# Kernel tuning notes

Measured on AMD Instinct MI355X. Metric: run time of the kernel, lower is better.

Reference implementation:

```python
import jax, jax.numpy as jnp
import numpy as np

H = 768       # hidden_size
NH = 12       # num_attention_heads
HD = H // NH  # head_size
FF = 3072     # intermediate_size
EPS = 1e-5


def _layernorm(x, g, b):
    m = jnp.mean(x, axis=-1, keepdims=True)
    v = jnp.var(x, axis=-1, keepdims=True)
    return (x - m) * jax.lax.rsqrt(v + EPS) * g + b


def setup_inputs() -> dict:
    key = jax.random.key(0)
    ks = jax.random.split(key, 12)
    B, Sq, Skv = 8, 1024, 1024
    s = 0.02
    return {
        "freq_hidden_states": jax.random.normal(ks[0], (B, Sq, H), jnp.float32),
        "image_hidden_states": jax.random.normal(ks[1], (B, Skv, H), jnp.float32),
        # attention projections (stored [in, out])
        "Wq": jax.random.normal(ks[2], (H, H), jnp.float32) * s,
        "bq": jnp.zeros((H,), jnp.float32),
        "Wk": jax.random.normal(ks[3], (H, H), jnp.float32) * s,
        "bk": jnp.zeros((H,), jnp.float32),
        "Wv": jax.random.normal(ks[4], (H, H), jnp.float32) * s,
        "bv": jnp.zeros((H,), jnp.float32),
        # layernorms
        "ln_att_g": jnp.ones((H,), jnp.float32),
        "ln_att_b": jnp.zeros((H,), jnp.float32),
        "ln_mlp_g": jnp.ones((H,), jnp.float32),
        "ln_mlp_b": jnp.zeros((H,), jnp.float32),
        # MLP
        "W1": jax.random.normal(ks[5], (H, FF), jnp.float32) * s,
        "b1": jnp.zeros((FF,), jnp.float32),
        "W2": jax.random.normal(ks[6], (FF, H), jnp.float32) * s,
        "b2": jnp.zeros((H,), jnp.float32),
    }


def reference(image_hidden_states, freq_hidden_states, Wq, bq, Wk, bk, Wv, bv,
              ln_att_g, ln_att_b, ln_mlp_g, ln_mlp_b, W1, b1, W2, b2):
    B, Sq, _ = freq_hidden_states.shape
    Skv = image_hidden_states.shape[1]
    # cross-attention: query from freq, key/value from image
    q = (freq_hidden_states @ Wq + bq).reshape(B, Sq, NH, HD)
    k = (image_hidden_states @ Wk + bk).reshape(B, Skv, NH, HD)
    v = (image_hidden_states @ Wv + bv).reshape(B, Skv, NH, HD)
    scores = jnp.einsum("bqhd,bkhd->bhqk", q, k) / jnp.sqrt(jnp.float32(HD))
    probs = jax.nn.softmax(scores, axis=-1)
    ctx = jnp.einsum("bhqk,bkhd->bqhd", probs, v).reshape(B, Sq, H)
    # residual with post-LN on the attention output
    h = freq_hidden_states + _layernorm(ctx, ln_att_g, ln_att_b)
    # MLP + residual with post-LN on the MLP output
    mlp = jax.nn.relu(h @ W1 + b1) @ W2 + b2
    return h + _layernorm(mlp, ln_mlp_g, ln_mlp_b)
```

## Files before the change

kernel.cpp:

```cpp
#include <hip/hip_runtime.h>
#include <hip/hip_bf16.h>

#define H 768
#define NH 12
#define HD 64
#define FF 3072
#define SQ 1024
#define SKV 1024

typedef __hip_bfloat16 bf16;
typedef __attribute__((ext_vector_type(8))) short short8;
typedef __attribute__((ext_vector_type(4))) float f32x4;

__device__ inline void gload16(const void* g, void* l) {
  __builtin_amdgcn_global_load_lds((const __attribute__((address_space(1))) void*)g,
                                   (__attribute__((address_space(3))) void*)l, 16, 0, 0);
}

__device__ inline float bf2f(unsigned short u) {
  unsigned int x = ((unsigned int)u) << 16;
  return __builtin_bit_cast(float, x);
}

__device__ inline void cvt_body(const float* __restrict__ src, bf16* __restrict__ dst, int blk) {
  int i = blk * 256 + threadIdx.x;
  float4 v = ((const float4*)src)[i];
  union { unsigned short u[4]; uint2 q; } o;
  bf16 t0 = __float2bfloat16(v.x); o.u[0] = *(unsigned short*)&t0;
  bf16 t1 = __float2bfloat16(v.y); o.u[1] = *(unsigned short*)&t1;
  bf16 t2 = __float2bfloat16(v.z); o.u[2] = *(unsigned short*)&t2;
  bf16 t3 = __float2bfloat16(v.w); o.u[3] = *(unsigned short*)&t3;
  ((uint2*)dst)[i] = o.q;
}

__device__ inline void trans_body(const float* __restrict__ src, bf16* __restrict__ dst,
                                  int Kd, int Nd, int blk, float* tile ) {
  int ntx = Nd >> 5;
  int n0 = (blk % ntx) << 5, k0 = (blk / ntx) << 5;
  int tx = threadIdx.x & 31, ty = threadIdx.x >> 5;
#pragma unroll
  for (int i = 0; i < 4; ++i)
    tile[(ty + i * 8) * 33 + tx] = src[(size_t)(k0 + ty + i * 8) * Nd + n0 + tx];
  __syncthreads();
#pragma unroll
  for (int i = 0; i < 4; ++i)
    dst[(size_t)(n0 + ty + i * 8) * Kd + k0 + tx] = __float2bfloat16(tile[tx * 33 + ty + i * 8]);
}

__global__ __launch_bounds__(256) void prep(
    const float* freq, const float* image, bf16* freqb, bf16* imageb,
    const float* Wq, const float* Wk, const float* Wv, const float* W1, const float* W2,
    bf16* WTq, bf16* WTk, bf16* WTv, bf16* W1T, bf16* W2T, int c1) {
  __shared__ float tile[32 * 33];
  int b = blockIdx.x;
  if (b < c1) { cvt_body(freq, freqb, b); return; }
  b -= c1;
  if (b < c1) { cvt_body(image, imageb, b); return; }
  b -= c1;
  const int TQ = (H / 32) * (H / 32);
  const int T1 = (FF / 32) * (H / 32);
  if (b < TQ)            { trans_body(Wq, WTq, H, H, b, tile); return; }
  b -= TQ;
  if (b < TQ)            { trans_body(Wk, WTk, H, H, b, tile); return; }
  b -= TQ;
  if (b < TQ)            { trans_body(Wv, WTv, H, H, b, tile); return; }
  b -= TQ;
  if (b < T1)            { trans_body(W1, W1T, H, FF, b, tile); return; }
  b -= T1;
  trans_body(W2, W2T, FF, H, b, tile);
}

template <int EPI, int BN>
__global__ __launch_bounds__(256) void gemm_bt(
    const bf16* __restrict__ A, const bf16* __restrict__ BT,
    const float* __restrict__ bias0, const float* __restrict__ bias1,
    void* __restrict__ out0, void* __restrict__ out1, int M, int N, int K) {
  constexpr int SI = BN / 32;
  constexpr int JF = BN / 32;
  __shared__ __align__(16) bf16 lA[128 * 64];
  __shared__ __align__(16) bf16 lB[BN * 64];
  const int t = threadIdx.x;
  const int lane = t & 63, w = t >> 6;
  const int wr = w >> 1, wc = w & 1;
  const int nt = N / BN;
  const int nwg = gridDim.x;
  int bid = blockIdx.x;
  int logical = ((nwg & 7) == 0) ? ((bid & 7) * (nwg >> 3) + (bid >> 3)) : bid;
  const int m0 = (logical / nt) << 7;
  const int n0 = (logical % nt) * BN;

  const f32x4 fz = {0.f, 0.f, 0.f, 0.f};
  f32x4 acc[4][JF];
#pragma unroll
  for (int i = 0; i < 4; ++i)
#pragma unroll
    for (int j = 0; j < JF; ++j) acc[i][j] = fz;

  for (int kt = 0; kt < K; kt += 64) {
#pragma unroll
    for (int i = 0; i < 4; ++i) {
      int idx = i * 256 + t;
      int row = idx >> 3;
      int chunk = (idx & 7) ^ (row & 7);
      gload16(A + (size_t)(m0 + row) * K + kt + chunk * 8, lA + (size_t)(i * 256 + w * 64) * 8);
    }
#pragma unroll
    for (int i = 0; i < SI; ++i) {
      int idx = i * 256 + t;
      int row = idx >> 3;
      int chunk = (idx & 7) ^ (row & 7);
      gload16(BT + (size_t)(n0 + row) * K + kt + chunk * 8, lB + (size_t)(i * 256 + w * 64) * 8);
    }
    __syncthreads();

    short8 af[2][4], bfv[2][JF];
#pragma unroll
    for (int s = 0; s < 2; ++s) {
#pragma unroll
      for (int i = 0; i < 4; ++i) {
        int ra = wr * 64 + i * 16 + (lane & 15);
        int ca = (s * 4 + (lane >> 4)) ^ (ra & 7);
        af[s][i] = *(const short8*)&lA[ra * 64 + ca * 8];
      }
#pragma unroll
      for (int j = 0; j < JF; ++j) {
        int rb = wc * (BN / 2) + j * 16 + (lane & 15);
        int cb = (s * 4 + (lane >> 4)) ^ (rb & 7);
        bfv[s][j] = *(const short8*)&lB[rb * 64 + cb * 8];
      }
    }
#pragma unroll
    for (int s = 0; s < 2; ++s)
#pragma unroll
      for (int i = 0; i < 4; ++i)
#pragma unroll
        for (int j = 0; j < JF; ++j)
          acc[i][j] = __builtin_amdgcn_mfma_f32_16x16x32_bf16(af[s][i], bfv[s][j], acc[i][j], 0, 0, 0);
    __syncthreads();
  }

#pragma unroll
  for (int i = 0; i < 4; ++i) {
    int mbase = m0 + wr * 64 + i * 16 + ((lane >> 4) << 2);
#pragma unroll
    for (int j = 0; j < JF; ++j) {
      int n = n0 + wc * (BN / 2) + j * 16 + (lane & 15);
#pragma unroll
      for (int r = 0; r < 4; ++r) {
        int m = mbase + r;
        float v = acc[i][j][r];
        if (EPI == 0) {
          v = (v + bias0[n]) * 0.180336880f;
          int hlin = (m >> 10) * NH + (n >> 6);
          ((bf16*)out0)[((size_t)hlin * SQ + (m & 1023)) * HD + (n & 63)] = __float2bfloat16(v);
        } else if (EPI == 1) {
          int sel = (n >= H);
          int nn = n - (sel ? H : 0);
          v += (sel ? bias1 : bias0)[nn];
          int hlin = (m >> 10) * NH + (nn >> 6);
          if (!sel)
            ((bf16*)out0)[((size_t)hlin * SKV + (m & 1023)) * HD + (nn & 63)] = __float2bfloat16(v);
          else
            ((bf16*)out1)[((size_t)hlin * HD + (nn & 63)) * SKV + (m & 1023)] = __float2bfloat16(v);
        } else if (EPI == 2) {
          v += bias0[n];
          v = fmaxf(v, 0.f);
          ((bf16*)out0)[(size_t)m * N + n] = __float2bfloat16(v);
        } else {
          v += bias0[n];
          ((bf16*)out0)[(size_t)m * N + n] = __float2bfloat16(v);
        }
      }
    }
  }
}

__global__ __launch_bounds__(512, 4) void attn_fwd(
    const bf16* __restrict__ Q,
    const bf16* __restrict__ Kg_,
    const bf16* __restrict__ VT,
    bf16* __restrict__ ctx, int nblk) {
  __shared__ __align__(16) bf16 Ks[2][64 * 64];
  __shared__ __align__(16) bf16 Vs[2][64 * 64];
  __shared__ __align__(16) bf16 PQ[8 * 16 * 72];

  const int t = threadIdx.x, lane = t & 63, w = t >> 6;
  int bid = blockIdx.x;
  int logical = ((nblk & 7) == 0) ? (bid & 7) * (nblk >> 3) + (bid >> 3) : bid;
  const int hl = logical >> 3;
  const int q0 = (logical & 7) << 7;
  const bf16* Qg = Q + ((size_t)hl * SQ + q0) * HD;
  const bf16* Kg = Kg_ + (size_t)hl * SKV * HD;
  const bf16* Vg = VT + (size_t)hl * HD * SKV;

#pragma unroll
  for (int rep = 0; rep < 2; ++rep) {
    int idx = rep * 512 + t;
    int row = idx >> 3;
    int chunk = (idx & 7) ^ (row & 7);
    gload16(Qg + (size_t)row * HD + chunk * 8, PQ + (size_t)(rep * 512 + w * 64) * 8);
  }
  {
    int row = t >> 3, chunk = (t & 7) ^ (row & 7);
    gload16(Kg + (size_t)row * HD + chunk * 8, &Ks[0][(size_t)w * 64 * 8]);
    gload16(Vg + (size_t)row * SKV + chunk * 8, &Vs[0][(size_t)w * 64 * 8]);
  }
  __syncthreads();

  short8 aq[2];
#pragma unroll
  for (int s = 0; s < 2; ++s) {
    int row = w * 16 + (lane & 15);
    int chunk = (s * 4 + (lane >> 4)) ^ (row & 7);
    aq[s] = *(const short8*)&PQ[row * 64 + chunk * 8];
  }
  __syncthreads();

  float l_r[4];
#pragma unroll
  for (int r = 0; r < 4; ++r) l_r[r] = 0.f;
  const f32x4 fz = {0.f, 0.f, 0.f, 0.f};
  f32x4 oacc[4];
#pragma unroll
  for (int j = 0; j < 4; ++j) oacc[j] = fz;

  bf16* Pw = PQ + w * (16 * 72);
  const short s1 = (short)0x3F80;
  const short8 ones = {s1, s1, s1, s1, s1, s1, s1, s1};

#pragma unroll 2
  for (int i = 0; i < 16; ++i) {
    const int buf = i & 1;
    if (i < 15) {
      int kvn = (i + 1) << 6;
      int row = t >> 3, chunk = (t & 7) ^ (row & 7);
      gload16(Kg + (size_t)(kvn + row) * HD + chunk * 8, &Ks[buf ^ 1][(size_t)w * 64 * 8]);
      gload16(Vg + (size_t)row * SKV + kvn + chunk * 8, &Vs[buf ^ 1][(size_t)w * 64 * 8]);
    }

    f32x4 sa[4];
#pragma unroll
    for (int n = 0; n < 4; ++n) sa[n] = fz;
    __builtin_amdgcn_s_setprio(1);
#pragma unroll
    for (int s = 0; s < 2; ++s)
#pragma unroll
      for (int n = 0; n < 4; ++n) {
        int rb = n * 16 + (lane & 15);
        int cb = (s * 4 + (lane >> 4)) ^ (rb & 7);
        short8 bk = *(const short8*)&Ks[buf][rb * 64 + cb * 8];
        sa[n] = __builtin_amdgcn_mfma_f32_16x16x32_bf16(aq[s], bk, sa[n], 0, 0, 0);
      }
    __builtin_amdgcn_s_setprio(0);

#pragma unroll
    for (int n = 0; n < 4; ++n)
#pragma unroll
      for (int r = 0; r < 4; ++r)
        Pw[(((lane >> 4) << 2) + r) * 72 + n * 16 + (lane & 15)] =
            __float2bfloat16(exp2f(sa[n][r]));

    f32x4 ld = fz;
    __builtin_amdgcn_s_setprio(1);
#pragma unroll
    for (int kk = 0; kk < 2; ++kk) {
      short8 pa = *(const short8*)&Pw[(lane & 15) * 72 + kk * 32 + ((lane >> 4) << 3)];
      ld = __builtin_amdgcn_mfma_f32_16x16x32_bf16(pa, ones, ld, 0, 0, 0);
#pragma unroll
      for (int j = 0; j < 4; ++j) {
        int rb = j * 16 + (lane & 15);
        int cb = (kk * 4 + (lane >> 4)) ^ (rb & 7);
        short8 bv = *(const short8*)&Vs[buf][rb * 64 + cb * 8];
        oacc[j] = __builtin_amdgcn_mfma_f32_16x16x32_bf16(pa, bv, oacc[j], 0, 0, 0);
      }
    }
    __builtin_amdgcn_s_setprio(0);
#pragma unroll
    for (int r = 0; r < 4; ++r) l_r[r] += ld[r];

    __syncthreads();
  }

  const int b = hl / NH, hh = hl % NH;
  float rl[4];
#pragma unroll
  for (int r = 0; r < 4; ++r) rl[r] = 1.0f / l_r[r];
#pragma unroll
  for (int j = 0; j < 4; ++j)
#pragma unroll
    for (int r = 0; r < 4; ++r) {
      int q = q0 + w * 16 + ((lane >> 4) << 2) + r;
      int d = j * 16 + (lane & 15);
      ctx[((size_t)b * SQ + q) * H + hh * HD + d] = __float2bfloat16(oacc[j][r] * rl[r]);
    }
}

__global__ __launch_bounds__(192) void ln_res(
    const bf16* __restrict__ x, const float* __restrict__ res,
    const float* __restrict__ g, const float* __restrict__ beta,
    float* __restrict__ o32, bf16* __restrict__ ob, int write_b) {
  const int row = blockIdx.x;
  const int t = threadIdx.x;
  float v[4];
  float s = 0.f, s2 = 0.f;
  ushort4 xv = ((const ushort4*)(x + (size_t)row * H))[t];
  v[0] = bf2f(xv.x); v[1] = bf2f(xv.y); v[2] = bf2f(xv.z); v[3] = bf2f(xv.w);
#pragma unroll
  for (int k = 0; k < 4; ++k) { s += v[k]; s2 += v[k] * v[k]; }
#pragma unroll
  for (int off = 32; off > 0; off >>= 1) {
    s += __shfl_down(s, off);
    s2 += __shfl_down(s2, off);
  }
  __shared__ float red[8];
  if ((t & 63) == 0) { red[t >> 6] = s; red[4 + (t >> 6)] = s2; }
  __syncthreads();
  float st = red[0] + red[1] + red[2];
  float s2t = red[4] + red[5] + red[6];
  float mean = st * (1.f / 768.f);
  float var = s2t * (1.f / 768.f) - mean * mean;
  float rs = rsqrtf(var + 1e-5f);
  {
    float4 rv = ((const float4*)(res + (size_t)row * H))[t];
    float4 gv = ((const float4*)g)[t];
    float4 bv = ((const float4*)beta)[t];
    float4 o;
    o.x = rv.x + (v[0] - mean) * rs * gv.x + bv.x;
    o.y = rv.y + (v[1] - mean) * rs * gv.y + bv.y;
    o.z = rv.z + (v[2] - mean) * rs * gv.z + bv.z;
    o.w = rv.w + (v[3] - mean) * rs * gv.w + bv.w;
    ((float4*)(o32 + (size_t)row * H))[t] = o;
    if (write_b) {
      union { unsigned short u[4]; uint2 q; } ob4;
      bf16 b0 = __float2bfloat16(o.x); ob4.u[0] = *(unsigned short*)&b0;
      bf16 b1 = __float2bfloat16(o.y); ob4.u[1] = *(unsigned short*)&b1;
      bf16 b2 = __float2bfloat16(o.z); ob4.u[2] = *(unsigned short*)&b2;
      bf16 b3 = __float2bfloat16(o.w); ob4.u[3] = *(unsigned short*)&b3;
      ((uint2*)(ob + (size_t)row * H))[t] = ob4.q;
    }
  }
}

extern "C" void kernel_launch(void* const* d_in, const int* in_sizes, int n_in,
                              void* d_out, int out_size, void* d_ws, size_t ws_size,
                              hipStream_t stream) {
  const float* freq  = (const float*)d_in[0];
  const float* image = (const float*)d_in[1];
  const float* Wq = (const float*)d_in[2];
  const float* bq = (const float*)d_in[3];
  const float* Wk = (const float*)d_in[4];
  const float* bk = (const float*)d_in[5];
  const float* Wv = (const float*)d_in[6];
  const float* bv = (const float*)d_in[7];
  const float* g1 = (const float*)d_in[8];
  const float* be1 = (const float*)d_in[9];
  const float* g2 = (const float*)d_in[10];
  const float* be2 = (const float*)d_in[11];
  const float* W1 = (const float*)d_in[12];
  const float* b1 = (const float*)d_in[13];
  const float* W2 = (const float*)d_in[14];
  const float* b2 = (const float*)d_in[15];

  const int Bc = in_sizes[0] / (SQ * H);
  const int M = Bc * SQ;

  char* p = (char*)d_ws;
  bf16* W1T = (bf16*)p;  p += (size_t)FF * H * 2;
  bf16* W2T = (bf16*)p;  p += (size_t)H * FF * 2;
  bf16* ctxb = (bf16*)p; p += (size_t)M * H * 2;
  float* h32 = (float*)p; p += (size_t)M * H * 4;
  bf16* hb = (bf16*)p;   p += (size_t)M * H * 2;
  char* U = p;
  bf16* freqb = (bf16*)U;
  bf16* imageb = (bf16*)(U + (size_t)M * H * 2);
  bf16* WTq   = (bf16*)(U + (size_t)2 * M * H * 2);
  bf16* WTkv  = (bf16*)(U + (size_t)2 * M * H * 2 + (size_t)H * H * 2);
  bf16* Qb    = (bf16*)(U + (size_t)2 * M * H * 2 + (size_t)3 * H * H * 2);
  bf16* Kbuf  = (bf16*)((char*)Qb + (size_t)M * H * 2);
  bf16* VTb   = (bf16*)((char*)Kbuf + (size_t)M * H * 2);
  bf16* mlp1  = (bf16*)U;
  bf16* mlp2b = ctxb;

  int c1 = M * H / 1024;
  int nprep = 2 * c1 + 3 * ((H / 32) * (H / 32)) + (FF / 32) * (H / 32) + (H / 32) * (FF / 32);
  prep<<<nprep, 256, 0, stream>>>(freq, image, freqb, imageb,
                                  Wq, Wk, Wv, W1, W2,
                                  WTq, WTkv, WTkv + (size_t)H * H, W1T, W2T, c1);

  gemm_bt<0, 64><<<(M / 128) * (H / 64), 256, 0, stream>>>(freqb, WTq, bq, nullptr, Qb, nullptr, M, H, H);
  gemm_bt<1, 128><<<(M / 128) * (2 * H / 128), 256, 0, stream>>>(imageb, WTkv, bk, bv, Kbuf, VTb, M, 2 * H, H);
  int nblk = Bc * NH * (SQ / 128);
  attn_fwd<<<nblk, 512, 0, stream>>>(Qb, Kbuf, VTb, ctxb, nblk);
  ln_res<<<M, 192, 0, stream>>>(ctxb, freq, g1, be1, h32, hb, 1);
  gemm_bt<2, 128><<<(M / 128) * (FF / 128), 256, 0, stream>>>(hb, W1T, b1, nullptr, mlp1, nullptr, M, FF, H);
  gemm_bt<3, 64><<<(M / 128) * (H / 64), 256, 0, stream>>>(mlp1, W2T, b2, nullptr, mlp2b, nullptr, M, H, FF);
  ln_res<<<M, 192, 0, stream>>>(mlp2b, h32, g2, be2, (float*)d_out, nullptr, 0);
}
```

Measured before the change: 247.2 us.

## Merge Q and KV projections into one launch and keep residuals in bf16

Fuses the Q projection GEMM into the K/V projection launch via a new epilogue mode that dispatches by block index. The V-transposed output is written as packed bf16 vectors. Both layernorm-residual kernels now read the residual from bf16 copies (freqb, hb) instead of fp32 tensors, which eliminates the fp32 intermediate h32 and its write/read traffic. This reduces launch count and memory bandwidth, at the cost of bf16 rounding of the residual path.

```diff
diff --git a/kernel.cpp b/kernel.cpp
--- a/kernel.cpp
+++ b/kernel.cpp
@@ -20,6 +20,12 @@
 __device__ inline float bf2f(unsigned short u) {
   unsigned int x = ((unsigned int)u) << 16;
   return __builtin_bit_cast(float, x);
+}
+
+__device__ inline unsigned int cvtpk(float lo, float hi) {
+  unsigned int r;
+  asm("v_cvt_pk_bf16_f32 %0, %1, %2" : "=v"(r) : "v"(lo), "v"(hi));
+  return r;
 }
 
 __device__ inline void cvt_body(const float* __restrict__ src, bf16* __restrict__ dst, int blk) {
@@ -74,7 +80,9 @@
 __global__ __launch_bounds__(256) void gemm_bt(
     const bf16* __restrict__ A, const bf16* __restrict__ BT,
     const float* __restrict__ bias0, const float* __restrict__ bias1,
-    void* __restrict__ out0, void* __restrict__ out1, int M, int N, int K) {
+    void* __restrict__ out0, void* __restrict__ out1, int M, int N, int K,
+    const bf16* __restrict__ Aq, const bf16* __restrict__ BTq,
+    const float* __restrict__ biasq, void* __restrict__ outq) {
   constexpr int SI = BN / 32;
   constexpr int JF = BN / 32;
   __shared__ __align__(16) bf16 lA[128 * 64];
@@ -82,12 +90,24 @@
   const int t = threadIdx.x;
   const int lane = t & 63, w = t >> 6;
   const int wr = w >> 1, wc = w & 1;
-  const int nt = N / BN;
   const int nwg = gridDim.x;
   int bid = blockIdx.x;
   int logical = ((nwg & 7) == 0) ? ((bid & 7) * (nwg >> 3) + (bid >> 3)) : bid;
-  const int m0 = (logical / nt) << 7;
-  const int n0 = (logical % nt) * BN;
+
+  bool isq = false;
+  int lg = logical;
+  const bf16* Ause = A;
+  const bf16* BTuse = BT;
+  int nt = N / BN;
+  if (EPI == 4) {
+    const int nkv = (M >> 7) * (2 * H / BN);
+    if (logical >= nkv) {
+      isq = true; lg = logical - nkv;
+      Ause = Aq; BTuse = BTq; nt = H / BN;
+    }
+  }
+  const int m0 = (lg / nt) << 7;
+  const int n0 = (lg % nt) * BN;
 
   const f32x4 fz = {0.f, 0.f, 0.f, 0.f};
   f32x4 acc[4][JF];
@@ -102,14 +122,14 @@
       int idx = i * 256 + t;
       int row = idx >> 3;
       int chunk = (idx & 7) ^ (row & 7);
-      gload16(A + (size_t)(m0 + row) * K + kt + chunk * 8, lA + (size_t)(i * 256 + w * 64) * 8);
+      gload16(Ause + (size_t)(m0 + row) * K + kt + chunk * 8, lA + (size_t)(i * 256 + w * 64) * 8);
     }
 #pragma unroll
     for (int i = 0; i < SI; ++i) {
       int idx = i * 256 + t;
       int row = idx >> 3;
       int chunk = (idx & 7) ^ (row & 7);
-      gload16(BT + (size_t)(n0 + row) * K + kt + chunk * 8, lB + (size_t)(i * 256 + w * 64) * 8);
+      gload16(BTuse + (size_t)(n0 + row) * K + kt + chunk * 8, lB + (size_t)(i * 256 + w * 64) * 8);
     }
     __syncthreads();
 
@@ -142,32 +162,44 @@
 #pragma unroll
   for (int i = 0; i < 4; ++i) {
     int mbase = m0 + wr * 64 + i * 16 + ((lane >> 4) << 2);
+    int mb = mbase & 1023, bidx = mbase >> 10;
 #pragma unroll
     for (int j = 0; j < JF; ++j) {
       int n = n0 + wc * (BN / 2) + j * 16 + (lane & 15);
-#pragma unroll
-      for (int r = 0; r < 4; ++r) {
-        int m = mbase + r;
-        float v = acc[i][j][r];
-        if (EPI == 0) {
-          v = (v + bias0[n]) * 0.180336880f;
-          int hlin = (m >> 10) * NH + (n >> 6);
-          ((bf16*)out0)[((size_t)hlin * SQ + (m & 1023)) * HD + (n & 63)] = __float2bfloat16(v);
-        } else if (EPI == 1) {
+      if (EPI == 4) {
+        if (isq) {
+          int hlin = bidx * NH + (n >> 6);
+#pragma unroll
+          for (int r = 0; r < 4; ++r) {
+            float v = (acc[i][j][r] + biasq[n]) * 0.180336880f;
+            ((bf16*)outq)[((size_t)hlin * SQ + (mb + r)) * HD + (n & 63)] = __float2bfloat16(v);
+          }
+        } else {
           int sel = (n >= H);
           int nn = n - (sel ? H : 0);
-          v += (sel ? bias1 : bias0)[nn];
-          int hlin = (m >> 10) * NH + (nn >> 6);
-          if (!sel)
-            ((bf16*)out0)[((size_t)hlin * SKV + (m & 1023)) * HD + (nn & 63)] = __float2bfloat16(v);
-          else
-            ((bf16*)out1)[((size_t)hlin * HD + (nn & 63)) * SKV + (m & 1023)] = __float2bfloat16(v);
-        } else if (EPI == 2) {
-          v += bias0[n];
-          v = fmaxf(v, 0.f);
-          ((bf16*)out0)[(size_t)m * N + n] = __float2bfloat16(v);
-        } else {
-          v += bias0[n];
+          int hlin = bidx * NH + (nn >> 6);
+          float bsv = (sel ? bias1 : bias0)[nn];
+          float v0 = acc[i][j][0] + bsv, v1 = acc[i][j][1] + bsv;
+          float v2 = acc[i][j][2] + bsv, v3 = acc[i][j][3] + bsv;
+          if (!sel) {
+            bf16* kp = (bf16*)out0 + ((size_t)hlin * SKV + mb) * HD + (nn & 63);
+            kp[0 * HD] = __float2bfloat16(v0);
+            kp[1 * HD] = __float2bfloat16(v1);
+            kp[2 * HD] = __float2bfloat16(v2);
+            kp[3 * HD] = __float2bfloat16(v3);
+          } else {
+            uint2 u;
+            u.x = cvtpk(v0, v1);
+            u.y = cvtpk(v2, v3);
+            *(uint2*)((bf16*)out1 + ((size_t)hlin * HD + (nn & 63)) * SKV + mb) = u;
+          }
+        }
+      } else {
+#pragma unroll
+        for (int r = 0; r < 4; ++r) {
+          int m = mbase + r;
+          float v = acc[i][j][r] + bias0[n];
+          if (EPI == 2) v = fmaxf(v, 0.f);
           ((bf16*)out0)[(size_t)m * N + n] = __float2bfloat16(v);
         }
       }
@@ -296,9 +328,9 @@
 }
 
 __global__ __launch_bounds__(192) void ln_res(
-    const bf16* __restrict__ x, const float* __restrict__ res,
+    const bf16* __restrict__ x, const bf16* __restrict__ res,
     const float* __restrict__ g, const float* __restrict__ beta,
-    float* __restrict__ o32, bf16* __restrict__ ob, int write_b) {
+    float* __restrict__ o32, bf16* __restrict__ ob) {
   const int row = blockIdx.x;
   const int t = threadIdx.x;
   float v[4];
@@ -321,22 +353,20 @@
   float var = s2t * (1.f / 768.f) - mean * mean;
   float rs = rsqrtf(var + 1e-5f);
   {
-    float4 rv = ((const float4*)(res + (size_t)row * H))[t];
+    ushort4 rv4 = ((const ushort4*)(res + (size_t)row * H))[t];
     float4 gv = ((const float4*)g)[t];
     float4 bv = ((const float4*)beta)[t];
     float4 o;
-    o.x = rv.x + (v[0] - mean) * rs * gv.x + bv.x;
-    o.y = rv.y + (v[1] - mean) * rs * gv.y + bv.y;
-    o.z = rv.z + (v[2] - mean) * rs * gv.z + bv.z;
-    o.w = rv.w + (v[3] - mean) * rs * gv.w + bv.w;
-    ((float4*)(o32 + (size_t)row * H))[t] = o;
-    if (write_b) {
-      union { unsigned short u[4]; uint2 q; } ob4;
-      bf16 b0 = __float2bfloat16(o.x); ob4.u[0] = *(unsigned short*)&b0;
-      bf16 b1 = __float2bfloat16(o.y); ob4.u[1] = *(unsigned short*)&b1;
-      bf16 b2 = __float2bfloat16(o.z); ob4.u[2] = *(unsigned short*)&b2;
-      bf16 b3 = __float2bfloat16(o.w); ob4.u[3] = *(unsigned short*)&b3;
-      ((uint2*)(ob + (size_t)row * H))[t] = ob4.q;
+    o.x = bf2f(rv4.x) + (v[0] - mean) * rs * gv.x + bv.x;
+    o.y = bf2f(rv4.y) + (v[1] - mean) * rs * gv.y + bv.y;
+    o.z = bf2f(rv4.z) + (v[2] - mean) * rs * gv.z + bv.z;
+    o.w = bf2f(rv4.w) + (v[3] - mean) * rs * gv.w + bv.w;
+    if (o32) ((float4*)(o32 + (size_t)row * H))[t] = o;
+    if (ob) {
+      uint2 q;
+      q.x = cvtpk(o.x, o.y);
+      q.y = cvtpk(o.z, o.w);
+      ((uint2*)(ob + (size_t)row * H))[t] = q;
     }
   }
 }
@@ -368,7 +398,6 @@
   bf16* W1T = (bf16*)p;  p += (size_t)FF * H * 2;
   bf16* W2T = (bf16*)p;  p += (size_t)H * FF * 2;
   bf16* ctxb = (bf16*)p; p += (size_t)M * H * 2;
-  float* h32 = (float*)p; p += (size_t)M * H * 4;
   bf16* hb = (bf16*)p;   p += (size_t)M * H * 2;
   char* U = p;
   bf16* freqb = (bf16*)U;
@@ -387,12 +416,15 @@
                                   Wq, Wk, Wv, W1, W2,
                                   WTq, WTkv, WTkv + (size_t)H * H, W1T, W2T, c1);
 
-  gemm_bt<0, 64><<<(M / 128) * (H / 64), 256, 0, stream>>>(freqb, WTq, bq, nullptr, Qb, nullptr, M, H, H);
-  gemm_bt<1, 128><<<(M / 128) * (2 * H / 128), 256, 0, stream>>>(imageb, WTkv, bk, bv, Kbuf, VTb, M, 2 * H, H);
+  int nqkv = (M / 128) * (2 * H / 128) + (M / 128) * (H / 128);
+  gemm_bt<4, 128><<<nqkv, 256, 0, stream>>>(imageb, WTkv, bk, bv, Kbuf, VTb, M, 2 * H, H,
+                                            freqb, WTq, bq, Qb);
   int nblk = Bc * NH * (SQ / 128);
   attn_fwd<<<nblk, 512, 0, stream>>>(Qb, Kbuf, VTb, ctxb, nblk);
-  ln_res<<<M, 192, 0, stream>>>(ctxb, freq, g1, be1, h32, hb, 1);
-  gemm_bt<2, 128><<<(M / 128) * (FF / 128), 256, 0, stream>>>(hb, W1T, b1, nullptr, mlp1, nullptr, M, FF, H);
-  gemm_bt<3, 64><<<(M / 128) * (H / 64), 256, 0, stream>>>(mlp1, W2T, b2, nullptr, mlp2b, nullptr, M, H, FF);
-  ln_res<<<M, 192, 0, stream>>>(mlp2b, h32, g2, be2, (float*)d_out, nullptr, 0);
-}
+  ln_res<<<M, 192, 0, stream>>>(ctxb, freqb, g1, be1, nullptr, hb);
+  gemm_bt<2, 128><<<(M / 128) * (FF / 128), 256, 0, stream>>>(hb, W1T, b1, nullptr, mlp1, nullptr,
+                                                              M, FF, H, nullptr, nullptr, nullptr, nullptr);
+  gemm_bt<3, 64><<<(M / 128) * (H / 64), 256, 0, stream>>>(mlp1, W2T, b2, nullptr, mlp2b, nullptr,
+                                                           M, H, FF, nullptr, nullptr, nullptr, nullptr);
+  ln_res<<<M, 192, 0, stream>>>(mlp2b, hb, g2, be2, (float*)d_out, nullptr);
+}
```

Result: faster. 230.6 us (-6.7%).
